# Kernel optimization log

Measured on AMD Instinct MI355X. Metric: run time of the kernel, lower is better.

The kernel has to match this reference:

```python
import jax, jax.numpy as jnp
import numpy as np

G, K = 1024, 16           # groups, agents per group
N, T, D = G * K, 32, 64   # total agents, timesteps, feature dim
LN_EPS = 1e-5


def setup_inputs() -> dict:
    key = jax.random.key(0)
    ks = jax.random.split(key, 6)
    x = jax.random.normal(ks[0], (N, T, D), dtype=jnp.float32)
    # one-hot group assignment [G, N]; agents grouped contiguously (matches repeat_interleave order)
    seg = jnp.repeat(jnp.arange(G), K)                      # [N]
    batch_traffic_id_map = jax.nn.one_hot(seg, G, dtype=jnp.float32).T  # [G, N]
    num_traffics = jnp.full((G,), K, dtype=jnp.int64) if jax.config.jax_enable_x64 else jnp.full((G,), K, dtype=jnp.int32)
    s = 1.0 / np.sqrt(D)
    fc1_w = jax.random.uniform(ks[1], (D, D), jnp.float32, -s, s)
    fc1_b = jax.random.uniform(ks[2], (D,), jnp.float32, -s, s)
    ln_w = jnp.ones((D,), jnp.float32)
    ln_b = jnp.zeros((D,), jnp.float32)
    fc2_w = jax.random.uniform(ks[3], (D, D), jnp.float32, -s, s)
    fc2_b = jax.random.uniform(ks[4], (D,), jnp.float32, -s, s)
    return {"x": x, "batch_traffic_id_map": batch_traffic_id_map,
            "num_traffics": num_traffics, "fc1_w": fc1_w, "fc1_b": fc1_b,
            "ln_w": ln_w, "ln_b": ln_b, "fc2_w": fc2_w, "fc2_b": fc2_b}


def _mlp(x, fc1_w, fc1_b, ln_w, ln_b, fc2_w, fc2_b):
    h = x @ fc1_w.T + fc1_b
    mu = jnp.mean(h, axis=-1, keepdims=True)
    var = jnp.mean((h - mu) ** 2, axis=-1, keepdims=True)
    h = (h - mu) * jax.lax.rsqrt(var + LN_EPS) * ln_w + ln_b
    h = jax.nn.relu(h)
    return h @ fc2_w.T + fc2_b


def reference(x, batch_traffic_id_map, num_traffics, fc1_w, fc1_b, ln_w, ln_b, fc2_w, fc2_b):
    h = _mlp(x, fc1_w, fc1_b, ln_w, ln_b, fc2_w, fc2_b)      # [N,T,D]
    # segment sum via dense one-hot matmul (same math as torch.matmul(map, x.transpose(0,1)))
    x2 = jnp.einsum('gn,tnd->tgd', batch_traffic_id_map, h.transpose(1, 0, 2))  # [T,G,D]
    counts = jnp.where(num_traffics == 0, 1, num_traffics).astype(x2.dtype)     # [G]
    x2 = x2 / counts[None, :, None]
    # broadcast group mean back to agents (repeat_interleave == gather by segment id)
    seg = jnp.argmax(batch_traffic_id_map, axis=0)            # [N]
    x2n = jnp.take(x2, seg, axis=1)                           # [T,N,D]
    return jnp.concatenate((x2n.transpose(1, 0, 2), h), axis=2)  # [N,T,2D]
```

## Files before the change

### kernel.cpp

```cpp
#include <hip/hip_runtime.h>


typedef __attribute__((ext_vector_type(8))) short bfrag_t;
typedef __attribute__((ext_vector_type(4))) float f4_t;

__device__ __forceinline__ short f2bf(float f) {
  union { float f; unsigned u; } v; v.f = f;
  unsigned r = v.u + 0x7fffu + ((v.u >> 16) & 1u);
  return (short)(r >> 16);
}

__device__ __forceinline__ bfrag_t load8_bf(const float* p) {
  const f4_t* q = reinterpret_cast<const f4_t*>(p);
  f4_t lo = q[0], hi = q[1];
  bfrag_t r;
  r[0] = f2bf(lo[0]); r[1] = f2bf(lo[1]); r[2] = f2bf(lo[2]); r[3] = f2bf(lo[3]);
  r[4] = f2bf(hi[0]); r[5] = f2bf(hi[1]); r[6] = f2bf(hi[2]); r[7] = f2bf(hi[3]);
  return r;
}

constexpr int T_ = 32;
constexpr int D_ = 64;
#define LN_EPS 1e-5f

__global__ __launch_bounds__(256) void sg_fused(
    const float* __restrict__ x,
    const int*   __restrict__ num_traffics,
    const float* __restrict__ w1, const float* __restrict__ b1,
    const float* __restrict__ lnw, const float* __restrict__ lnb,
    const float* __restrict__ w2, const float* __restrict__ b2,
    float* __restrict__ out)
{
  __shared__ short lds_h[4][16 * 64];

  const int tid  = threadIdx.x;
  const int wave = tid >> 6;
  const int lane = tid & 63;
  const int m    = lane & 15;
  const int quad = lane >> 4;

  const int g     = blockIdx.x >> 1;
  const int thalf = blockIdx.x & 1;

  bfrag_t wf1[2][4], wf2[2][4];
  #pragma unroll
  for (int kk = 0; kk < 2; ++kk)
    #pragma unroll
    for (int tau = 0; tau < 4; ++tau) {
      wf1[kk][tau] = load8_bf(w1 + (tau*16 + m)*D_ + kk*32 + quad*8);
      wf2[kk][tau] = load8_bf(w2 + (tau*16 + m)*D_ + kk*32 + quad*8);
    }

  float bias1[4], bias2[4], lw[4], lb[4];
  #pragma unroll
  for (int tau = 0; tau < 4; ++tau) {
    bias1[tau] = b1[tau*16 + m];
    bias2[tau] = b2[tau*16 + m];
    lw[tau]    = lnw[tau*16 + m];
    lb[tau]    = lnb[tau*16 + m];
  }
  int cnt = num_traffics[g];
  if (cnt == 0) cnt = 1;
  const float inv_cnt = 1.0f / (float)cnt;

  short* myld = lds_h[wave];

  for (int it = 0; it < 4; ++it) {
    const int t = thalf*16 + wave*4 + it;

    const float* xrow = x + ((size_t)(g*16 + m) * T_ + t) * D_;
    bfrag_t af0 = load8_bf(xrow + 0*32 + quad*8);
    bfrag_t af1 = load8_bf(xrow + 1*32 + quad*8);

    f4_t acc[4];
    #pragma unroll
    for (int tau = 0; tau < 4; ++tau) {
      f4_t c = {0.f, 0.f, 0.f, 0.f};
      c = __builtin_amdgcn_mfma_f32_16x16x32_bf16(af0, wf1[0][tau], c, 0, 0, 0);
      c = __builtin_amdgcn_mfma_f32_16x16x32_bf16(af1, wf1[1][tau], c, 0, 0, 0);
      acc[tau] = c;
    }

    float s[4] = {0,0,0,0}, sq[4] = {0,0,0,0};
    #pragma unroll
    for (int tau = 0; tau < 4; ++tau)
      #pragma unroll
      for (int i = 0; i < 4; ++i) {
        float v = acc[tau][i] + bias1[tau];
        acc[tau][i] = v;
        s[i] += v; sq[i] += v * v;
      }
    #pragma unroll
    for (int mask = 1; mask < 16; mask <<= 1)
      #pragma unroll
      for (int i = 0; i < 4; ++i) {
        s[i]  += __shfl_xor(s[i],  mask, 64);
        sq[i] += __shfl_xor(sq[i], mask, 64);
      }
    float mu[4], rs[4];
    #pragma unroll
    for (int i = 0; i < 4; ++i) {
      mu[i] = s[i] * (1.0f / 64.0f);
      float var = sq[i] * (1.0f / 64.0f) - mu[i]*mu[i];
      rs[i] = rsqrtf(var + LN_EPS);
    }

    #pragma unroll
    for (int tau = 0; tau < 4; ++tau)
      #pragma unroll
      for (int i = 0; i < 4; ++i) {
        float v = (acc[tau][i] - mu[i]) * rs[i] * lw[tau] + lb[tau];
        v = fmaxf(v, 0.0f);
        myld[(quad*4 + i)*64 + tau*16 + m] = f2bf(v);
      }

    bfrag_t hf0 = *reinterpret_cast<const bfrag_t*>(&myld[m*64 + 0*32 + quad*8]);
    bfrag_t hf1 = *reinterpret_cast<const bfrag_t*>(&myld[m*64 + 1*32 + quad*8]);

    f4_t acc2[4];
    #pragma unroll
    for (int tau = 0; tau < 4; ++tau) {
      f4_t c = {0.f, 0.f, 0.f, 0.f};
      c = __builtin_amdgcn_mfma_f32_16x16x32_bf16(hf0, wf2[0][tau], c, 0, 0, 0);
      c = __builtin_amdgcn_mfma_f32_16x16x32_bf16(hf1, wf2[1][tau], c, 0, 0, 0);
      acc2[tau] = c;
    }

    float csum[4];
    #pragma unroll
    for (int tau = 0; tau < 4; ++tau) {
      float t0 = 0.f;
      #pragma unroll
      for (int i = 0; i < 4; ++i) {
        float v = acc2[tau][i] + bias2[tau];
        acc2[tau][i] = v;
        t0 += v;
      }
      csum[tau] = t0;
    }
    #pragma unroll
    for (int mask = 16; mask < 64; mask <<= 1)
      #pragma unroll
      for (int tau = 0; tau < 4; ++tau)
        csum[tau] += __shfl_xor(csum[tau], mask, 64);
    float mean[4];
    #pragma unroll
    for (int tau = 0; tau < 4; ++tau) mean[tau] = csum[tau] * inv_cnt;

    #pragma unroll
    for (int i = 0; i < 4; ++i) {
      const size_t base = ((size_t)(g*16 + quad*4 + i) * T_ + t) * (2*D_);
      #pragma unroll
      for (int tau = 0; tau < 4; ++tau) {
        out[base + tau*16 + m]      = mean[tau];
        out[base + 64 + tau*16 + m] = acc2[tau][i];
      }
    }
  }
}

extern "C" void kernel_launch(void* const* d_in, const int* in_sizes, int n_in,
                              void* d_out, int out_size, void* d_ws, size_t ws_size,
                              hipStream_t stream) {
  const float* x   = (const float*)d_in[0];
  const int*   ntr = (const int*)d_in[2];
  const float* w1  = (const float*)d_in[3];
  const float* b1  = (const float*)d_in[4];
  const float* lnw = (const float*)d_in[5];
  const float* lnb = (const float*)d_in[6];
  const float* w2  = (const float*)d_in[7];
  const float* b2  = (const float*)d_in[8];
  float* out = (float*)d_out;

  dim3 grid(2048), block(256);
  hipLaunchKernelGGL(sg_fused, grid, block, 0, stream,
                     x, ntr, w1, b1, lnw, lnb, w2, b2, out);
}
```

Before: 414.4 us.

## Stage bf16 weights in LDS once per block, use packed cvt and nontemporal IO

Only wave 0 now loads and converts the two weight matrices to bf16, storing them in shared memory. All waves then read MFMA B-fragments from LDS instead of each wave loading and converting its own copy into registers. Conversions use the packed bf16 hardware builtin when it is available. x loads and output stores become nontemporal, and launch bounds request 4 blocks per CU. This lowers per-wave global weight traffic and register pressure, at the cost of a block barrier and LDS reads inside the loop.

```diff
diff --git a/kernel.cpp b/kernel.cpp
--- a/kernel.cpp
+++ b/kernel.cpp
@@ -4,26 +4,41 @@
 typedef __attribute__((ext_vector_type(8))) short bfrag_t;
 typedef __attribute__((ext_vector_type(4))) float f4_t;
 
-__device__ __forceinline__ short f2bf(float f) {
-  union { float f; unsigned u; } v; v.f = f;
-  unsigned r = v.u + 0x7fffu + ((v.u >> 16) & 1u);
-  return (short)(r >> 16);
-}
-
-__device__ __forceinline__ bfrag_t load8_bf(const float* p) {
-  const f4_t* q = reinterpret_cast<const f4_t*>(p);
-  f4_t lo = q[0], hi = q[1];
-  bfrag_t r;
-  r[0] = f2bf(lo[0]); r[1] = f2bf(lo[1]); r[2] = f2bf(lo[2]); r[3] = f2bf(lo[3]);
-  r[4] = f2bf(hi[0]); r[5] = f2bf(hi[1]); r[6] = f2bf(hi[2]); r[7] = f2bf(hi[3]);
-  return r;
+__device__ __forceinline__ unsigned pkbf(float a, float b) {
+#if defined(__has_builtin)
+#if __has_builtin(__builtin_amdgcn_cvt_pk_bf16_f32)
+  auto r = __builtin_amdgcn_cvt_pk_bf16_f32(a, b);
+  union { decltype(r) v; unsigned u; } c; c.v = r; return c.u;
+#define PKBF_DONE 1
+#endif
+#endif
+#ifndef PKBF_DONE
+  union { float f; unsigned u; } va, vb;
+  va.f = a; vb.f = b;
+  unsigned ra = va.u + 0x7fffu + ((va.u >> 16) & 1u);
+  unsigned rb = vb.u + 0x7fffu + ((vb.u >> 16) & 1u);
+  return (ra >> 16) | (rb & 0xffff0000u);
+#endif
+}
+
+__device__ __forceinline__ short f2bf1(float a) {
+  return (short)(unsigned short)(pkbf(a, a) & 0xffffu);
+}
+
+__device__ __forceinline__ bfrag_t cvt8(f4_t lo, f4_t hi) {
+  union { bfrag_t f; unsigned u[4]; } c;
+  c.u[0] = pkbf(lo[0], lo[1]);
+  c.u[1] = pkbf(lo[2], lo[3]);
+  c.u[2] = pkbf(hi[0], hi[1]);
+  c.u[3] = pkbf(hi[2], hi[3]);
+  return c.f;
 }
 
 constexpr int T_ = 32;
 constexpr int D_ = 64;
 #define LN_EPS 1e-5f
 
-__global__ __launch_bounds__(256) void sg_fused(
+__global__ __launch_bounds__(256, 4) void sg_fused(
     const float* __restrict__ x,
     const int*   __restrict__ num_traffics,
     const float* __restrict__ w1, const float* __restrict__ b1,
@@ -31,7 +46,8 @@
     const float* __restrict__ w2, const float* __restrict__ b2,
     float* __restrict__ out)
 {
-  __shared__ short lds_h[4][16 * 64];
+  __shared__ short   lds_h[4][16 * 64];
+  __shared__ bfrag_t wlds[2][2][4][64];
 
   const int tid  = threadIdx.x;
   const int wave = tid >> 6;
@@ -42,14 +58,20 @@
   const int g     = blockIdx.x >> 1;
   const int thalf = blockIdx.x & 1;
 
-  bfrag_t wf1[2][4], wf2[2][4];
-  #pragma unroll
-  for (int kk = 0; kk < 2; ++kk)
-    #pragma unroll
-    for (int tau = 0; tau < 4; ++tau) {
-      wf1[kk][tau] = load8_bf(w1 + (tau*16 + m)*D_ + kk*32 + quad*8);
-      wf2[kk][tau] = load8_bf(w2 + (tau*16 + m)*D_ + kk*32 + quad*8);
-    }
+  if (wave == 0) {
+    #pragma unroll
+    for (int mat = 0; mat < 2; ++mat) {
+      const float* w = mat ? w2 : w1;
+      #pragma unroll
+      for (int kk = 0; kk < 2; ++kk)
+        #pragma unroll
+        for (int tau = 0; tau < 4; ++tau) {
+          const float* p = w + (tau*16 + m)*D_ + kk*32 + quad*8;
+          const f4_t* q = reinterpret_cast<const f4_t*>(p);
+          wlds[mat][kk][tau][lane] = cvt8(q[0], q[1]);
+        }
+    }
+  }
 
   float bias1[4], bias2[4], lw[4], lb[4];
   #pragma unroll
@@ -63,21 +85,29 @@
   if (cnt == 0) cnt = 1;
   const float inv_cnt = 1.0f / (float)cnt;
 
+  __syncthreads();
+
   short* myld = lds_h[wave];
 
   for (int it = 0; it < 4; ++it) {
     const int t = thalf*16 + wave*4 + it;
 
     const float* xrow = x + ((size_t)(g*16 + m) * T_ + t) * D_;
-    bfrag_t af0 = load8_bf(xrow + 0*32 + quad*8);
-    bfrag_t af1 = load8_bf(xrow + 1*32 + quad*8);
+    const f4_t* xq = reinterpret_cast<const f4_t*>(xrow + quad*8);
+    f4_t x0 = __builtin_nontemporal_load(xq);
+    f4_t x1 = __builtin_nontemporal_load(xq + 1);
+    const f4_t* xq2 = reinterpret_cast<const f4_t*>(xrow + 32 + quad*8);
+    f4_t x2 = __builtin_nontemporal_load(xq2);
+    f4_t x3 = __builtin_nontemporal_load(xq2 + 1);
+    bfrag_t af0 = cvt8(x0, x1);
+    bfrag_t af1 = cvt8(x2, x3);
 
     f4_t acc[4];
     #pragma unroll
     for (int tau = 0; tau < 4; ++tau) {
       f4_t c = {0.f, 0.f, 0.f, 0.f};
-      c = __builtin_amdgcn_mfma_f32_16x16x32_bf16(af0, wf1[0][tau], c, 0, 0, 0);
-      c = __builtin_amdgcn_mfma_f32_16x16x32_bf16(af1, wf1[1][tau], c, 0, 0, 0);
+      c = __builtin_amdgcn_mfma_f32_16x16x32_bf16(af0, wlds[0][0][tau][lane], c, 0, 0, 0);
+      c = __builtin_amdgcn_mfma_f32_16x16x32_bf16(af1, wlds[0][1][tau][lane], c, 0, 0, 0);
       acc[tau] = c;
     }
 
@@ -111,7 +141,7 @@
       for (int i = 0; i < 4; ++i) {
         float v = (acc[tau][i] - mu[i]) * rs[i] * lw[tau] + lb[tau];
         v = fmaxf(v, 0.0f);
-        myld[(quad*4 + i)*64 + tau*16 + m] = f2bf(v);
+        myld[(quad*4 + i)*64 + tau*16 + m] = f2bf1(v);
       }
 
     bfrag_t hf0 = *reinterpret_cast<const bfrag_t*>(&myld[m*64 + 0*32 + quad*8]);
@@ -121,8 +151,8 @@
     #pragma unroll
     for (int tau = 0; tau < 4; ++tau) {
       f4_t c = {0.f, 0.f, 0.f, 0.f};
-      c = __builtin_amdgcn_mfma_f32_16x16x32_bf16(hf0, wf2[0][tau], c, 0, 0, 0);
-      c = __builtin_amdgcn_mfma_f32_16x16x32_bf16(hf1, wf2[1][tau], c, 0, 0, 0);
+      c = __builtin_amdgcn_mfma_f32_16x16x32_bf16(hf0, wlds[1][0][tau][lane], c, 0, 0, 0);
+      c = __builtin_amdgcn_mfma_f32_16x16x32_bf16(hf1, wlds[1][1][tau][lane], c, 0, 0, 0);
       acc2[tau] = c;
     }
 
@@ -152,8 +182,8 @@
       const size_t base = ((size_t)(g*16 + quad*4 + i) * T_ + t) * (2*D_);
       #pragma unroll
       for (int tau = 0; tau < 4; ++tau) {
-        out[base + tau*16 + m]      = mean[tau];
-        out[base + 64 + tau*16 + m] = acc2[tau][i];
+        __builtin_nontemporal_store(mean[tau],    out + base + tau*16 + m);
+        __builtin_nontemporal_store(acc2[tau][i], out + base + 64 + tau*16 + m);
       }
     }
   }
```

New measurement: 407.3 us. Within noise of the previous version (-1.7%).
